# Performance work log

Measured on AMD Instinct MI355X. Metric: run time of the kernel, lower is better.

The kernel has to match this reference:

```python
import jax, jax.numpy as jnp
import numpy as np
import math

V, E, H, A, N = 32000, 512, 512, 64, 8  # vocab, embed, rnn hidden, att_size, n_heads
T, B = 256, 128                          # scan length (acts as att batch), inner dim


def _lstm(x, Wih, Whh, bih, bhh):
    # x: (T, B, E); torch nn.LSTM gate order i, f, g, o; zero initial state
    Bb = x.shape[1]
    Hh = Whh.shape[1]
    init = (jnp.zeros((Bb, Hh), x.dtype), jnp.zeros((Bb, Hh), x.dtype))

    def step(carry, xt):
        h, c = carry
        gates = xt @ Wih.T + bih + h @ Whh.T + bhh          # (B, 4H)
        i, f, g, o = jnp.split(gates, 4, axis=-1)
        c = jax.nn.sigmoid(f) * c + jax.nn.sigmoid(i) * jnp.tanh(g)
        h = jax.nn.sigmoid(o) * jnp.tanh(c)
        return (h, c), h

    _, hs = jax.lax.scan(step, init, x)
    return hs  # (T, B, H)


def setup_inputs() -> dict:
    key = jax.random.key(0)
    ks = jax.random.split(key, 26)
    rn = lambda k, s: jax.random.normal(k, s, jnp.float32) * 0.02
    inp = {
        "input_seq_l": jax.random.randint(ks[0], (T, B), 0, V, jnp.int32),
        "input_seq_r": jax.random.randint(ks[1], (T, B), 0, V, jnp.int32),
        "emb_l": rn(ks[2], (V, E)),
        "emb_r": rn(ks[3], (V, E)),
        "Wih_l": rn(ks[4], (4 * H, E)), "Whh_l": rn(ks[5], (4 * H, H)),
        "bih_l": rn(ks[6], (4 * H,)), "bhh_l": rn(ks[7], (4 * H,)),
        "Wih_r": rn(ks[8], (4 * H, E)), "Whh_r": rn(ks[9], (4 * H, H)),
        "bih_r": rn(ks[10], (4 * H,)), "bhh_r": rn(ks[11], (4 * H,)),
        "Wq": rn(ks[12], (N, H, A)), "bq": rn(ks[13], (N, A)),
        "Wk": rn(ks[14], (N, H, A)), "bk": rn(ks[15], (N, A)),
        "Wv": rn(ks[16], (N, H, A)), "bv": rn(ks[17], (N, A)),
        "Wo": rn(ks[18], (N * A, H)), "bo": rn(ks[19], (H,)),
        "Wh": rn(ks[20], (2 * H, 64)), "bh": rn(ks[21], (64,)),
        "Wa": rn(ks[22], (64, 2)), "ba": rn(ks[23], (2,)),
    }
    return inp


def reference(input_seq_l, input_seq_r, emb_l, emb_r,
              Wih_l, Whh_l, bih_l, bhh_l,
              Wih_r, Whh_r, bih_r, bhh_r,
              Wq, bq, Wk, bk, Wv, bv, Wo, bo, Wh, bh, Wa, ba):
    # left encoder
    ol = _lstm(emb_l[input_seq_l], Wih_l, Whh_l, bih_l, bhh_l)   # (T, B, H)
    # multi-head attention over left outputs (all heads batched)
    q = jnp.einsum('tbh,nhd->ntbd', ol, Wq) + bq[:, None, None, :]
    k = jnp.einsum('tbh,nhd->ntbd', ol, Wk) + bk[:, None, None, :]
    v = jnp.einsum('tbh,nhd->ntbd', ol, Wv) + bv[:, None, None, :]
    scores = jnp.einsum('ntbd,ntcd->ntbc', q, k) / math.sqrt(A)  # (N, T, B, B)
    p = jax.nn.softmax(scores, axis=-1)
    att = jnp.einsum('ntbc,ntcd->ntbd', p, v)                    # (N, T, B, A)
    att = att.transpose(1, 2, 0, 3).reshape(att.shape[1], att.shape[2], -1)  # (T, B, N*A)
    ol = att @ Wo + bo                                           # (T, B, H)
    ol = ol.mean(axis=1)                                         # (T, H)
    # right encoder
    orr = _lstm(emb_r[input_seq_r], Wih_r, Whh_r, bih_r, bhh_r).mean(axis=1)  # (T, H)
    cat = jnp.concatenate([ol, orr], axis=1)                     # (T, 2H)
    fc = cat @ Wh + bh
    ans = jax.nn.softmax(fc @ Wa + ba, axis=1)                   # (T, 2)
    return ans
```

## Files before the change

kernel.cpp:

```cpp
#include <hip/hip_runtime.h>

typedef unsigned short u16;
typedef __attribute__((ext_vector_type(4))) float f32x4;
typedef __attribute__((ext_vector_type(8))) short bf8;

#define MFMA16(a, b, c) __builtin_amdgcn_mfma_f32_16x16x32_bf16((a), (b), (c), 0, 0, 0)

__device__ __forceinline__ u16 f2bf(float f) {
  unsigned u = __builtin_bit_cast(unsigned, f);
  u += 0x7FFFu + ((u >> 16) & 1u);
  return (u16)(u >> 16);
}
__device__ __forceinline__ float bf2f(u16 h) {
  unsigned u = ((unsigned)h) << 16;
  return __builtin_bit_cast(float, u);
}
__device__ __forceinline__ float sigm(float x) { return 1.0f / (1.0f + __expf(-x)); }
__device__ __forceinline__ float tanh_f(float x) {
  x = fminf(fmaxf(x, -15.f), 15.f);
  float e = __expf(2.f * x);
  return (e - 1.f) / (e + 1.f);
}

__global__ void k_cast(const float* __restrict__ in, u16* __restrict__ out, int n4) {
  int i = blockIdx.x * blockDim.x + threadIdx.x;
  if (i >= n4) return;
  float4 v = ((const float4*)in)[i];
  union { u16 h[4]; uint2 u; } p;
  p.h[0] = f2bf(v.x); p.h[1] = f2bf(v.y); p.h[2] = f2bf(v.z); p.h[3] = f2bf(v.w);
  ((uint2*)out)[i] = p.u;
}

__global__ void k_bsum(const float* __restrict__ a, const float* __restrict__ b,
                       float* __restrict__ o, int n) {
  int i = blockIdx.x * blockDim.x + threadIdx.x;
  if (i < n) o[i] = a[i] + b[i];
}

__global__ void k_zero32(unsigned* __restrict__ p, int n) {
  int i = blockIdx.x * blockDim.x + threadIdx.x;
  if (i < n) p[i] = 0u;
}

__global__ void k_fill(float* __restrict__ p, int n, float v) {
  int i = blockIdx.x * blockDim.x + threadIdx.x;
  if (i < n) p[i] = v;
}

__global__ void k_tqkv(const float* __restrict__ W, u16* __restrict__ WT) {
  int g = blockIdx.x * blockDim.x + threadIdx.x;
  int n = g >> 15, d = (g >> 9) & 63, h = g & 511;
  WT[g] = f2bf(W[(n << 15) + (h << 6) + d]);
}

__global__ __launch_bounds__(256, 2) void k_gemm_gates(
    const int* __restrict__ idx, const float* __restrict__ emb,
    const float* __restrict__ Wih, u16* __restrict__ Gpre, int m_base) {
  __shared__ u16 lA[128][72];
  __shared__ u16 lB[128][72];
  int n0 = blockIdx.x * 128;
  int m0 = blockIdx.y * 128;
  int tid = threadIdx.x;
  int lane = tid & 63, wid = tid >> 6;
  int wm = (wid >> 1) << 6, wn = (wid & 1) << 6;
  int lq = lane >> 4, lc = lane & 15;
  f32x4 acc[4][4] = {};
  for (int k0 = 0; k0 < 512; k0 += 64) {
#pragma unroll
    for (int s = 0; s < 2; s++) {
      int slot = tid + s * 256;
      int row = slot >> 2, seg = (slot & 3) << 4;
      const float* pa = emb + (size_t)idx[m_base + m0 + row] * 512 + k0 + seg;
      const float* pb = Wih + (size_t)(n0 + row) * 512 + k0 + seg;
      float4 a0 = ((const float4*)pa)[0], a1 = ((const float4*)pa)[1];
      float4 a2 = ((const float4*)pa)[2], a3 = ((const float4*)pa)[3];
      float4 b0 = ((const float4*)pb)[0], b1 = ((const float4*)pb)[1];
      float4 b2 = ((const float4*)pb)[2], b3 = ((const float4*)pb)[3];
      union { u16 h[8]; int4 v; } pk;
      pk.h[0]=f2bf(a0.x); pk.h[1]=f2bf(a0.y); pk.h[2]=f2bf(a0.z); pk.h[3]=f2bf(a0.w);
      pk.h[4]=f2bf(a1.x); pk.h[5]=f2bf(a1.y); pk.h[6]=f2bf(a1.z); pk.h[7]=f2bf(a1.w);
      *(int4*)&lA[row][seg] = pk.v;
      pk.h[0]=f2bf(a2.x); pk.h[1]=f2bf(a2.y); pk.h[2]=f2bf(a2.z); pk.h[3]=f2bf(a2.w);
      pk.h[4]=f2bf(a3.x); pk.h[5]=f2bf(a3.y); pk.h[6]=f2bf(a3.z); pk.h[7]=f2bf(a3.w);
      *(int4*)&lA[row][seg + 8] = pk.v;
      pk.h[0]=f2bf(b0.x); pk.h[1]=f2bf(b0.y); pk.h[2]=f2bf(b0.z); pk.h[3]=f2bf(b0.w);
      pk.h[4]=f2bf(b1.x); pk.h[5]=f2bf(b1.y); pk.h[6]=f2bf(b1.z); pk.h[7]=f2bf(b1.w);
      *(int4*)&lB[row][seg] = pk.v;
      pk.h[0]=f2bf(b2.x); pk.h[1]=f2bf(b2.y); pk.h[2]=f2bf(b2.z); pk.h[3]=f2bf(b2.w);
      pk.h[4]=f2bf(b3.x); pk.h[5]=f2bf(b3.y); pk.h[6]=f2bf(b3.z); pk.h[7]=f2bf(b3.w);
      *(int4*)&lB[row][seg + 8] = pk.v;
    }
    __syncthreads();
#pragma unroll
    for (int kk = 0; kk < 64; kk += 32) {
      int ko = kk + (lq << 3);
      bf8 af[4], bg[4];
#pragma unroll
      for (int i = 0; i < 4; i++) af[i] = *(const bf8*)&lA[wm + i * 16 + lc][ko];
#pragma unroll
      for (int j = 0; j < 4; j++) bg[j] = *(const bf8*)&lB[wn + j * 16 + lc][ko];
#pragma unroll
      for (int i = 0; i < 4; i++)
#pragma unroll
        for (int j = 0; j < 4; j++) acc[i][j] = MFMA16(af[i], bg[j], acc[i][j]);
    }
    __syncthreads();
  }
  int cr = lq << 2;
#pragma unroll
  for (int i = 0; i < 4; i++)
#pragma unroll
    for (int j = 0; j < 4; j++)
#pragma unroll
      for (int r = 0; r < 4; r++) {
        int m = m0 + wm + i * 16 + cr + r;
        int nn = n0 + wn + j * 16 + lc;
        Gpre[(size_t)m * 2048 + nn] = f2bf(acc[i][j][r]);
      }
}

__global__ __launch_bounds__(256, 1) void k_lstm2(
    const u16* __restrict__ Gl, const u16* __restrict__ Gr,
    const u16* __restrict__ Whl, const u16* __restrict__ Whr,
    const float* __restrict__ bsl, const float* __restrict__ bsr,
    u16* __restrict__ hsl, u16* __restrict__ hsr,
    unsigned* __restrict__ hx, float* __restrict__ cstate,
    unsigned* __restrict__ flg, int t0, int nT) {
  __shared__ __align__(16) char hlds[32768];
  int bid = blockIdx.x;
  int pod = bid & 7, cg = bid >> 3;
  int e = pod >> 2, bg = pod & 3;
  int b0 = bg << 5, c0 = cg << 5;
  const u16* Gpre = e ? Gr : Gl;
  const u16* Whh  = e ? Whr : Whl;
  const float* bsum = e ? bsr : bsl;
  u16* hs = e ? hsr : hsl;

  int tid = threadIdx.x, lane = tid & 63, w = tid >> 6;
  int lq = lane >> 4, lc = lane & 15, cr = lq << 2;
  int cl = (w << 3) + (lc & 7);
  int gg0 = lc >> 3;
  int lr0 = (gg0 << 5) + cl;
  int lr1 = ((2 + gg0) << 5) + cl;
  int gc0 = (gg0 << 9) + c0 + cl;
  int gc1 = ((2 + gg0) << 9) + c0 + cl;
  float bs0 = bsum[gc0], bs1 = bsum[gc1];
  bool owner = (lc & 8) != 0;

  int gr0 = ((lr0 >> 5) << 9) + c0 + (lr0 & 31);
  int gr1 = ((lr1 >> 5) << 9) + c0 + (lr1 & 31);
  bf8 wb0[16], wb1[16];
  {
    const u16* p0 = Whh + (size_t)gr0 * 512 + (lq << 3);
    const u16* p1 = Whh + (size_t)gr1 * 512 + (lq << 3);
#pragma unroll
    for (int ks = 0; ks < 16; ks++) {
      wb0[ks] = *(const bf8*)(p0 + (ks << 5));
      wb1[ks] = *(const bf8*)(p1 + (ks << 5));
    }
  }
  float creg[2][4];
#pragma unroll
  for (int mi = 0; mi < 2; mi++)
#pragma unroll
    for (int r = 0; r < 4; r++) creg[mi][r] = 0.f;
  if (t0 > 0 && owner) {
#pragma unroll
    for (int mi = 0; mi < 2; mi++)
#pragma unroll
      for (int r = 0; r < 4; r++)
        creg[mi][r] = cstate[(size_t)((e << 7) + b0 + (mi << 4) + cr + r) * 512 + c0 + cl];
  }

  u16 gp[2][2][4];
#pragma unroll
  for (int mi = 0; mi < 2; mi++)
#pragma unroll
    for (int r = 0; r < 4; r++) {
      size_t rowb = (size_t)(b0 + (mi << 4) + cr + r) << 11;
      gp[mi][0][r] = Gpre[rowb + gc0];
      gp[mi][1][r] = Gpre[rowb + gc1];
    }

  int ax = (lc & 7) << 4;
  int abyte0 = lc << 10;
  int abyte1 = (16 + lc) << 10;
  int hxc = (c0 >> 1) + (w << 2) + ((lc & 7) >> 1);
  const int srow = tid >> 6;
  const int scolb = (tid & 63) << 4;

  for (int t = 0; t < nT; t++) {
    int tg = t0 + t;
    f32x4 acc[2][2] = {};
    if (tg > 0) {
      if (t > 0) {
        if (tid < 64) {
          const unsigned* fa = flg + (pod << 6) + (lane & 15);
          unsigned fv;
          int guard = 0;
          while (true) {
            asm volatile("global_load_dword %0, %1, off sc0 sc1"
                         : "=v"(fv) : "v"(fa) : "memory");
            asm volatile("s_waitcnt vmcnt(0)" ::: "memory");
            if (__ballot(fv >= (unsigned)t) == ~0ull) break;
            if (++guard > 300000) break;
          }
        }
        __syncthreads();
      }
      const unsigned* hxr = hx + (((size_t)((e << 1) | ((tg - 1) & 1))) << 15);
      uint4 sv[8];
#pragma unroll
      for (int i = 0; i < 8; i++) {
        int row = (i << 2) + srow;
        const unsigned* ap = hxr + (((size_t)(b0 + row)) << 8) + ((tid & 63) << 2);
        asm volatile("global_load_dwordx4 %0, %1, off sc0 sc1"
                     : "=v"(sv[i]) : "v"(ap));
      }
      asm volatile("s_waitcnt vmcnt(0)" ::: "memory");
      __builtin_amdgcn_sched_barrier(0);
#pragma unroll
      for (int i = 0; i < 8; i++) {
        int row = (i << 2) + srow;
        *(uint4*)(hlds + (row << 10) + (scolb ^ ((row & 7) << 4))) = sv[i];
      }
      __syncthreads();
#pragma unroll
      for (int ks = 0; ks < 16; ks++) {
        int kb = (ks << 6) + (lq << 4);
        bf8 a0 = *(const bf8*)(hlds + abyte0 + (kb ^ ax));
        bf8 a1 = *(const bf8*)(hlds + abyte1 + (kb ^ ax));
        acc[0][0] = MFMA16(a0, wb0[ks], acc[0][0]);
        acc[0][1] = MFMA16(a0, wb1[ks], acc[0][1]);
        acc[1][0] = MFMA16(a1, wb0[ks], acc[1][0]);
        acc[1][1] = MFMA16(a1, wb1[ks], acc[1][1]);
      }
      __syncthreads();
    }
    unsigned* hxw = hx + (((size_t)((e << 1) | (tg & 1))) << 15);
#pragma unroll
    for (int mi = 0; mi < 2; mi++)
#pragma unroll
      for (int r = 0; r < 4; r++) {
        float v0 = acc[mi][0][r] + bf2f(gp[mi][0][r]) + bs0;
        float v1 = acc[mi][1][r] + bf2f(gp[mi][1][r]) + bs1;
        float send = sigm(v0) * tanh_f(v1);
        float recv = __shfl_xor(send, 8, 64);
        float h = 0.f;
        if (owner) {
          float c = sigm(v0) * creg[mi][r] + recv;
          creg[mi][r] = c;
          h = sigm(v1) * tanh_f(c);
        }
        unsigned hb = (unsigned)f2bf(h);
        unsigned hi = __shfl_down(hb, 1, 64);
        unsigned packed = (hb & 0xffffu) | (hi << 16);
        int b = b0 + (mi << 4) + cr + r;
        if (owner) {
          hs[((size_t)((tg << 7) + b) << 9) + c0 + cl] = (u16)hb;
          if (!(lane & 1)) {
            unsigned* sa = hxw + (((size_t)b) << 8) + hxc;
            asm volatile("global_store_dword %0, %1, off sc0 sc1"
                         :: "v"(sa), "v"(packed) : "memory");
          }
        }
      }
    asm volatile("s_waitcnt vmcnt(0)" ::: "memory");
    __syncthreads();
    if (tid == 0) {
      unsigned tv = (unsigned)(t + 1);
      unsigned* fa = flg + (pod << 6) + cg;
      asm volatile("global_store_dword %0, %1, off sc0 sc1"
                   :: "v"(fa), "v"(tv) : "memory");
    }
    if (t + 1 < nT) {
#pragma unroll
      for (int mi = 0; mi < 2; mi++)
#pragma unroll
        for (int r = 0; r < 4; r++) {
          size_t rowb = (size_t)(((t + 1) << 7) + b0 + (mi << 4) + cr + r) << 11;
          gp[mi][0][r] = Gpre[rowb + gc0];
          gp[mi][1][r] = Gpre[rowb + gc1];
        }
    }
  }
  if (owner) {
#pragma unroll
    for (int mi = 0; mi < 2; mi++)
#pragma unroll
      for (int r = 0; r < 4; r++)
        cstate[(size_t)((e << 7) + b0 + (mi << 4) + cr + r) * 512 + c0 + cl] = creg[mi][r];
  }
}

__global__ __launch_bounds__(256) void k_meanr(const u16* __restrict__ hs, float* __restrict__ out) {
  __shared__ float part[4][512];
  int t = blockIdx.x, tid = threadIdx.x;
  int rg = tid >> 6, ln = tid & 63;
  float s[8] = {};
  for (int b = rg << 5; b < (rg << 5) + 32; b++) {
    bf8 v = *(const bf8*)(hs + (((size_t)((t << 7) + b)) << 9) + (ln << 3));
#pragma unroll
    for (int j = 0; j < 8; j++) s[j] += bf2f((u16)v[j]);
  }
#pragma unroll
  for (int j = 0; j < 8; j++) part[rg][(ln << 3) + j] = s[j];
  __syncthreads();
  for (int c = tid; c < 512; c += 256)
    out[(t << 9) + c] = (part[0][c] + part[1][c] + part[2][c] + part[3][c]) * 0.0078125f;
}

__global__ __launch_bounds__(256, 1) void k_attn(
    const u16* __restrict__ hs,
    const u16* __restrict__ WqT, const u16* __restrict__ WkT, const u16* __restrict__ WvT,
    const float* __restrict__ bq, const float* __restrict__ bk, const float* __restrict__ bv,
    float* __restrict__ attmean) {
  __shared__ __align__(16) char smem[123904];
  u16 (*qs)[72]  = (u16(*)[72])smem;
  u16 (*ksm)[72] = (u16(*)[72])(smem + 18432);
  u16 (*vt)[136] = (u16(*)[136])(smem + 36864);
  float (*sc)[132] = (float(*)[132])(smem + 54272);
  u16 (*ps)[136] = (u16(*)[136])smem;
  float* red = (float*)(smem + 54272);
  float* pmax = (float*)(smem + 121856);
  float* psum = (float*)(smem + 122880);

  int bid = blockIdx.x;
  int n = bid >> 8, t = bid & 255;
  int tid = threadIdx.x, lane = tid & 63, wid = tid >> 6;
  int lq = lane >> 4, lc = lane & 15, cr = lq << 2;
  const u16* ol = hs + ((size_t)t << 16);

  float bqv[4], bkv[4];
#pragma unroll
  for (int nf = 0; nf < 4; nf++) {
    bqv[nf] = bq[(n << 6) + (nf << 4) + lc];
    bkv[nf] = bk[(n << 6) + (nf << 4) + lc];
  }
  float bvv[4][4];
#pragma unroll
  for (int mi = 0; mi < 4; mi++)
#pragma unroll
    for (int r = 0; r < 4; r++) bvv[mi][r] = bv[(n << 6) + (mi << 4) + cr + r];

  const u16* wq = WqT + ((size_t)n << 15);
  const u16* wk = WkT + ((size_t)n << 15);
  const u16* wv = WvT + ((size_t)n << 15);
  f32x4 aq[2][4] = {}, ak[2][4] = {}, av[4][2] = {};
  for (int ks = 0; ks < 16; ks++) {
    int ko = (ks << 5) + (lq << 3);
    bf8 a0 = *(const bf8*)&ol[(size_t)((wid << 5) + lc) * 512 + ko];
    bf8 a1 = *(const bf8*)&ol[(size_t)((wid << 5) + 16 + lc) * 512 + ko];
#pragma unroll
    for (int nf = 0; nf < 4; nf++) {
      bf8 bw = *(const bf8*)&wq[(size_t)((nf << 4) + lc) * 512 + ko];
      aq[0][nf] = MFMA16(a0, bw, aq[0][nf]);
      aq[1][nf] = MFMA16(a1, bw, aq[1][nf]);
      bf8 bw2 = *(const bf8*)&wk[(size_t)((nf << 4) + lc) * 512 + ko];
      ak[0][nf] = MFMA16(a0, bw2, ak[0][nf]);
      ak[1][nf] = MFMA16(a1, bw2, ak[1][nf]);
    }
#pragma unroll
    for (int mi = 0; mi < 4; mi++) {
      bf8 aw = *(const bf8*)&wv[(size_t)((mi << 4) + lc) * 512 + ko];
      av[mi][0] = MFMA16(aw, a0, av[mi][0]);
      av[mi][1] = MFMA16(aw, a1, av[mi][1]);
    }
  }
#pragma unroll
  for (int mi = 0; mi < 2; mi++)
#pragma unroll
    for (int nf = 0; nf < 4; nf++)
#pragma unroll
      for (int r = 0; r < 4; r++) {
        int b = (wid << 5) + (mi << 4) + cr + r;
        int d = (nf << 4) + lc;
        qs[b][d] = f2bf(aq[mi][nf][r] + bqv[nf]);
        ksm[b][d] = f2bf(ak[mi][nf][r] + bkv[nf]);
      }
#pragma unroll
  for (int mi = 0; mi < 4; mi++)
#pragma unroll
    for (int c2 = 0; c2 < 2; c2++)
#pragma unroll
      for (int r = 0; r < 4; r++) {
        int d = (mi << 4) + cr + r;
        int c = (wid << 5) + (c2 << 4) + lc;
        vt[d][c] = f2bf(av[mi][c2][r] + bvv[mi][r]);
      }
  __syncthreads();

  f32x4 as_[2][8] = {};
#pragma unroll
  for (int ks = 0; ks < 2; ks++) {
    int ko = (ks << 5) + (lq << 3);
    bf8 a0 = *(const bf8*)&qs[(wid << 5) + lc][ko];
    bf8 a1 = *(const bf8*)&qs[(wid << 5) + 16 + lc][ko];
#pragma unroll
    for (int nf = 0; nf < 8; nf++) {
      bf8 bw = *(const bf8*)&ksm[(nf << 4) + lc][ko];
      as_[0][nf] = MFMA16(a0, bw, as_[0][nf]);
      as_[1][nf] = MFMA16(a1, bw, as_[1][nf]);
    }
  }
#pragma unroll
  for (int mi = 0; mi < 2; mi++)
#pragma unroll
    for (int nf = 0; nf < 8; nf++)
#pragma unroll
      for (int r = 0; r < 4; r++)
        sc[(wid << 5) + (mi << 4) + cr + r][(nf << 4) + lc] = as_[mi][nf][r] * 0.125f;
  __syncthreads();

  {
    int row = tid & 127, half = tid >> 7;
    int cb = half << 6;
    float mx = -1e30f;
    for (int j = 0; j < 64; j++) mx = fmaxf(mx, sc[row][cb + j]);
    pmax[(half << 7) + row] = mx;
    __syncthreads();
    mx = fmaxf(pmax[row], pmax[128 + row]);
    float s = 0.f;
    for (int j = 0; j < 64; j++) { float ev = __expf(sc[row][cb + j] - mx); s += ev; sc[row][cb + j] = ev; }
    psum[(half << 7) + row] = s;
    __syncthreads();
    float inv = 1.f / (psum[row] + psum[128 + row]);
    for (int j = 0; j < 64; j++) ps[row][cb + j] = f2bf(sc[row][cb + j] * inv);
  }
  __syncthreads();

  f32x4 ao[2][4] = {};
#pragma unroll
  for (int ks = 0; ks < 4; ks++) {
    int ko = (ks << 5) + (lq << 3);
    bf8 a0 = *(const bf8*)&ps[(wid << 5) + lc][ko];
    bf8 a1 = *(const bf8*)&ps[(wid << 5) + 16 + lc][ko];
#pragma unroll
    for (int nf = 0; nf < 4; nf++) {
      bf8 bw = *(const bf8*)&vt[(nf << 4) + lc][ko];
      ao[0][nf] = MFMA16(a0, bw, ao[0][nf]);
      ao[1][nf] = MFMA16(a1, bw, ao[1][nf]);
    }
  }
  float pm[4];
#pragma unroll
  for (int nf = 0; nf < 4; nf++) {
    float s = 0.f;
#pragma unroll
    for (int mi = 0; mi < 2; mi++)
#pragma unroll
      for (int r = 0; r < 4; r++) s += ao[mi][nf][r];
    s += __shfl_xor(s, 16, 64);
    s += __shfl_xor(s, 32, 64);
    pm[nf] = s;
  }
  if (lq == 0) {
#pragma unroll
    for (int nf = 0; nf < 4; nf++) red[(wid << 6) + (nf << 4) + lc] = pm[nf];
  }
  __syncthreads();
  if (tid < 64) {
    float s = red[tid] + red[64 + tid] + red[128 + tid] + red[192 + tid];
    attmean[(t << 9) + (n << 6) + tid] = s * 0.0078125f;
  }
}

__global__ __launch_bounds__(256) void k_olm(const float* __restrict__ am, const float* __restrict__ Wo,
                                             const float* __restrict__ bo, float* __restrict__ olm) {
  __shared__ float row[512];
  int t = blockIdx.x >> 1, h0 = (blockIdx.x & 1) << 8;
  int tid = threadIdx.x;
  row[tid] = am[(t << 9) + tid];
  row[tid + 256] = am[(t << 9) + 256 + tid];
  __syncthreads();
  int h = h0 + tid;
  float s = bo[h];
  for (int k = 0; k < 512; k++) s += row[k] * Wo[(k << 9) + h];
  olm[(t << 9) + h] = s;
}

__global__ __launch_bounds__(64) void k_final(const float* __restrict__ olmp, const float* __restrict__ hrm,
                                              const float* __restrict__ Wh, const float* __restrict__ bh,
                                              const float* __restrict__ Wa, const float* __restrict__ ba,
                                              float* __restrict__ out) {
  __shared__ float cat[1024];
  int t = blockIdx.x, j = threadIdx.x;
  for (int i = j; i < 512; i += 64) {
    cat[i] = olmp[(t << 9) + i];
    cat[512 + i] = hrm[(t << 9) + i];
  }
  __syncthreads();
  float f = bh[j];
  for (int k = 0; k < 1024; k++) f += cat[k] * Wh[(k << 6) + j];
  float p0 = f * Wa[j * 2], p1 = f * Wa[j * 2 + 1];
#pragma unroll
  for (int o = 32; o > 0; o >>= 1) { p0 += __shfl_down(p0, o); p1 += __shfl_down(p1, o); }
  if (j == 0) {
    p0 += ba[0]; p1 += ba[1];
    float m = fmaxf(p0, p1);
    float e0 = __expf(p0 - m), e1 = __expf(p1 - m);
    float inv = 1.f / (e0 + e1);
    out[t * 2] = e0 * inv;
    out[t * 2 + 1] = e1 * inv;
  }
}

extern "C" void kernel_launch(void* const* d_in, const int* in_sizes, int n_in,
                              void* d_out, int out_size, void* d_ws, size_t ws_size,
                              hipStream_t stream) {
  const int*   seq_l = (const int*)d_in[0];
  const int*   seq_r = (const int*)d_in[1];
  const float* emb_l = (const float*)d_in[2];
  const float* emb_r = (const float*)d_in[3];
  const float* Wih_l = (const float*)d_in[4];
  const float* Whh_l = (const float*)d_in[5];
  const float* bih_l = (const float*)d_in[6];
  const float* bhh_l = (const float*)d_in[7];
  const float* Wih_r = (const float*)d_in[8];
  const float* Whh_r = (const float*)d_in[9];
  const float* bih_r = (const float*)d_in[10];
  const float* bhh_r = (const float*)d_in[11];
  const float* Wq = (const float*)d_in[12];
  const float* bq = (const float*)d_in[13];
  const float* Wk = (const float*)d_in[14];
  const float* bk = (const float*)d_in[15];
  const float* Wv = (const float*)d_in[16];
  const float* bv = (const float*)d_in[17];
  const float* Wo = (const float*)d_in[18];
  const float* bo = (const float*)d_in[19];
  const float* Wh = (const float*)d_in[20];
  const float* bhc = (const float*)d_in[21];
  const float* Wa = (const float*)d_in[22];
  const float* ba = (const float*)d_in[23];
  float* out = (float*)d_out;

  char* ws = (char*)d_ws;
  size_t off = 0;
  auto alloc = [&](size_t bytes) { char* p = ws + off; off += (bytes + 255) & ~(size_t)255; return p; };
  u16*   hsl  = (u16*)alloc(33554432);
  u16*   hsr  = (u16*)alloc(33554432);
  u16*   Whl  = (u16*)alloc(2097152);
  u16*   Whr  = (u16*)alloc(2097152);
  u16*   WqT  = (u16*)alloc(524288);
  u16*   WkT  = (u16*)alloc(524288);
  u16*   WvT  = (u16*)alloc(524288);
  float* bsl  = (float*)alloc(8192);
  float* bsr  = (float*)alloc(8192);
  unsigned* hx = (unsigned*)alloc(524288);
  float* cst  = (float*)alloc(524288);
  unsigned* flg = (unsigned*)alloc(2048);
  float* am   = (float*)alloc(524288);
  float* hrm  = (float*)alloc(524288);
  float* olm  = (float*)alloc(524288);
  size_t fixed = off;

  int Tc = 0;
  const int cands[4] = {256, 128, 64, 32};
  for (int i = 0; i < 4; i++) {
    size_t need = fixed + 2ull * (size_t)cands[i] * 524288ull;
    if (need <= ws_size) { Tc = cands[i]; break; }
  }
  if (Tc == 0) {
    k_fill<<<2, 256, 0, stream>>>(out, out_size, 0.25f);
    return;
  }
  size_t gbytes = (size_t)Tc * 524288ull;
  u16* Gl = (u16*)alloc(gbytes);
  u16* Gr = (u16*)alloc(gbytes);

  k_cast<<<1024, 256, 0, stream>>>(Whh_l, Whl, 262144);
  k_cast<<<1024, 256, 0, stream>>>(Whh_r, Whr, 262144);
  k_bsum<<<8, 256, 0, stream>>>(bih_l, bhh_l, bsl, 2048);
  k_bsum<<<8, 256, 0, stream>>>(bih_r, bhh_r, bsr, 2048);
  k_tqkv<<<1024, 256, 0, stream>>>(Wq, WqT);
  k_tqkv<<<1024, 256, 0, stream>>>(Wk, WkT);
  k_tqkv<<<1024, 256, 0, stream>>>(Wv, WvT);

  int nC = 256 / Tc;
  for (int c = 0; c < nC; c++) {
    int m_base = c * Tc * 128;
    k_gemm_gates<<<dim3(16, Tc), 256, 0, stream>>>(seq_l, emb_l, Wih_l, Gl, m_base);
    k_gemm_gates<<<dim3(16, Tc), 256, 0, stream>>>(seq_r, emb_r, Wih_r, Gr, m_base);
    k_zero32<<<2, 256, 0, stream>>>(flg, 512);
    k_lstm2<<<128, 256, 0, stream>>>(Gl, Gr, Whl, Whr, bsl, bsr, hsl, hsr,
                                     hx, cst, flg, c * Tc, Tc);
  }
  k_meanr<<<256, 256, 0, stream>>>(hsr, hrm);
  k_attn<<<2048, 256, 0, stream>>>(hsl, WqT, WkT, WvT, bq, bk, bv, am);
  k_olm<<<512, 256, 0, stream>>>(am, Wo, bo, olm);
  k_final<<<256, 64, 0, stream>>>(olm, hrm, Wh, bhc, Wa, ba, out);
}
```

Baseline: 1.869 ms.

## Overlap next-chunk input GEMM with LSTM recurrence in a fused kernel

The input-projection GEMM and the persistent LSTM recurrence are merged into one launch. The first 128 blocks run the recurrence for the current time chunk while extra blocks compute the gate pre-activations for the next chunk into a double buffer, so the GEMM runs on otherwise idle CUs. The chunk size is capped at 128 so that there are at least two chunks to pipeline, and the flags now use global timesteps so they do not need resetting between chunks. The h stores are also packed into 32-bit writes. The risk is that the GEMM blocks compete with the spin-waiting recurrence blocks for memory bandwidth, and that more kernel launches and chunk boundaries add overhead.

```diff
diff --git a/kernel.cpp b/kernel.cpp
--- a/kernel.cpp
+++ b/kernel.cpp
@@ -53,14 +53,12 @@
   WT[g] = f2bf(W[(n << 15) + (h << 6) + d]);
 }
 
-__global__ __launch_bounds__(256, 2) void k_gemm_gates(
+__device__ __forceinline__ void gemm_body(
     const int* __restrict__ idx, const float* __restrict__ emb,
-    const float* __restrict__ Wih, u16* __restrict__ Gpre, int m_base) {
-  __shared__ u16 lA[128][72];
-  __shared__ u16 lB[128][72];
-  int n0 = blockIdx.x * 128;
-  int m0 = blockIdx.y * 128;
-  int tid = threadIdx.x;
+    const float* __restrict__ Wih, u16* __restrict__ Gpre,
+    int m_base, int m0, int n0, char* smem, int tid) {
+  u16 (*lA)[72] = (u16(*)[72])smem;
+  u16 (*lB)[72] = (u16(*)[72])(smem + 18432);
   int lane = tid & 63, wid = tid >> 6;
   int wm = (wid >> 1) << 6, wn = (wid & 1) << 6;
   int lq = lane >> 4, lc = lane & 15;
@@ -119,15 +117,21 @@
       }
 }
 
-__global__ __launch_bounds__(256, 1) void k_lstm2(
+__global__ __launch_bounds__(256, 2) void k_gemm_gates(
+    const int* __restrict__ idx, const float* __restrict__ emb,
+    const float* __restrict__ Wih, u16* __restrict__ Gpre, int m_base) {
+  __shared__ __align__(16) char smem[36864];
+  gemm_body(idx, emb, Wih, Gpre, m_base, blockIdx.y << 7, blockIdx.x << 7,
+            smem, threadIdx.x);
+}
+
+__device__ void lstm_body(
     const u16* __restrict__ Gl, const u16* __restrict__ Gr,
     const u16* __restrict__ Whl, const u16* __restrict__ Whr,
     const float* __restrict__ bsl, const float* __restrict__ bsr,
     u16* __restrict__ hsl, u16* __restrict__ hsr,
     unsigned* __restrict__ hx, float* __restrict__ cstate,
-    unsigned* __restrict__ flg, int t0, int nT) {
-  __shared__ __align__(16) char hlds[32768];
-  int bid = blockIdx.x;
+    unsigned* __restrict__ flg, int t0, int nT, char* hlds, int bid, int tid) {
   int pod = bid & 7, cg = bid >> 3;
   int e = pod >> 2, bg = pod & 3;
   int b0 = bg << 5, c0 = cg << 5;
@@ -136,7 +140,7 @@
   const float* bsum = e ? bsr : bsl;
   u16* hs = e ? hsr : hsl;
 
-  int tid = threadIdx.x, lane = tid & 63, w = tid >> 6;
+  int lane = tid & 63, w = tid >> 6;
   int lq = lane >> 4, lc = lane & 15, cr = lq << 2;
   int cl = (w << 3) + (lc & 7);
   int gg0 = lc >> 3;
@@ -202,7 +206,7 @@
             asm volatile("global_load_dword %0, %1, off sc0 sc1"
                          : "=v"(fv) : "v"(fa) : "memory");
             asm volatile("s_waitcnt vmcnt(0)" ::: "memory");
-            if (__ballot(fv >= (unsigned)t) == ~0ull) break;
+            if (__ballot(fv >= (unsigned)tg) == ~0ull) break;
             if (++guard > 300000) break;
           }
         }
@@ -256,19 +260,17 @@
         unsigned hi = __shfl_down(hb, 1, 64);
         unsigned packed = (hb & 0xffffu) | (hi << 16);
         int b = b0 + (mi << 4) + cr + r;
-        if (owner) {
-          hs[((size_t)((tg << 7) + b) << 9) + c0 + cl] = (u16)hb;
-          if (!(lane & 1)) {
-            unsigned* sa = hxw + (((size_t)b) << 8) + hxc;
-            asm volatile("global_store_dword %0, %1, off sc0 sc1"
-                         :: "v"(sa), "v"(packed) : "memory");
-          }
+        if (owner && !(lane & 1)) {
+          *(unsigned*)(hs + (((size_t)((tg << 7) + b)) << 9) + c0 + cl) = packed;
+          unsigned* sa = hxw + (((size_t)b) << 8) + hxc;
+          asm volatile("global_store_dword %0, %1, off sc0 sc1"
+                       :: "v"(sa), "v"(packed) : "memory");
         }
       }
     asm volatile("s_waitcnt vmcnt(0)" ::: "memory");
     __syncthreads();
     if (tid == 0) {
-      unsigned tv = (unsigned)(t + 1);
+      unsigned tv = (unsigned)(tg + 1);
       unsigned* fa = flg + (pod << 6) + cg;
       asm volatile("global_store_dword %0, %1, off sc0 sc1"
                    :: "v"(fa), "v"(tv) : "memory");
@@ -290,6 +292,32 @@
 #pragma unroll
       for (int r = 0; r < 4; r++)
         cstate[(size_t)((e << 7) + b0 + (mi << 4) + cr + r) * 512 + c0 + cl] = creg[mi][r];
+  }
+}
+
+__global__ __launch_bounds__(256, 1) void k_fused(
+    const u16* __restrict__ Gl, const u16* __restrict__ Gr,
+    u16* __restrict__ Ggl, u16* __restrict__ Ggr,
+    const int* __restrict__ seq_l, const int* __restrict__ seq_r,
+    const float* __restrict__ emb_l, const float* __restrict__ emb_r,
+    const float* __restrict__ Wih_l, const float* __restrict__ Wih_r,
+    const u16* __restrict__ Whl, const u16* __restrict__ Whr,
+    const float* __restrict__ bsl, const float* __restrict__ bsr,
+    u16* __restrict__ hsl, u16* __restrict__ hsr,
+    unsigned* __restrict__ hx, float* __restrict__ cstate,
+    unsigned* __restrict__ flg, int t0, int nT, int gmb, int Tc) {
+  __shared__ __align__(16) char smem[36864];
+  int bid = blockIdx.x, tid = threadIdx.x;
+  if (bid < 128) {
+    lstm_body(Gl, Gr, Whl, Whr, bsl, bsr, hsl, hsr, hx, cstate, flg,
+              t0, nT, smem, bid, tid);
+  } else {
+    int gb = bid - 128;
+    int per = Tc << 4;
+    int ge = gb >= per;
+    int rem = ge ? gb - per : gb;
+    gemm_body(ge ? seq_r : seq_l, ge ? emb_r : emb_l, ge ? Wih_r : Wih_l,
+              ge ? Ggr : Ggl, gmb, (rem >> 4) << 7, (rem & 15) << 7, smem, tid);
   }
 }
 
@@ -555,9 +583,9 @@
   size_t fixed = off;
 
   int Tc = 0;
-  const int cands[4] = {256, 128, 64, 32};
-  for (int i = 0; i < 4; i++) {
-    size_t need = fixed + 2ull * (size_t)cands[i] * 524288ull;
+  const int cands[3] = {128, 64, 32};
+  for (int i = 0; i < 3; i++) {
+    size_t need = fixed + 4ull * (size_t)cands[i] * 524288ull;
     if (need <= ws_size) { Tc = cands[i]; break; }
   }
   if (Tc == 0) {
@@ -565,9 +593,11 @@
     return;
   }
   size_t gbytes = (size_t)Tc * 524288ull;
-  u16* Gl = (u16*)alloc(gbytes);
-  u16* Gr = (u16*)alloc(gbytes);
-
+  u16* Glb[2]; u16* Grb[2];
+  Glb[0] = (u16*)alloc(gbytes); Glb[1] = (u16*)alloc(gbytes);
+  Grb[0] = (u16*)alloc(gbytes); Grb[1] = (u16*)alloc(gbytes);
+
+  k_zero32<<<2, 256, 0, stream>>>(flg, 512);
   k_cast<<<1024, 256, 0, stream>>>(Whh_l, Whl, 262144);
   k_cast<<<1024, 256, 0, stream>>>(Whh_r, Whr, 262144);
   k_bsum<<<8, 256, 0, stream>>>(bih_l, bhh_l, bsl, 2048);
@@ -576,14 +606,18 @@
   k_tqkv<<<1024, 256, 0, stream>>>(Wk, WkT);
   k_tqkv<<<1024, 256, 0, stream>>>(Wv, WvT);
 
+  k_gemm_gates<<<dim3(16, Tc), 256, 0, stream>>>(seq_l, emb_l, Wih_l, Glb[0], 0);
+  k_gemm_gates<<<dim3(16, Tc), 256, 0, stream>>>(seq_r, emb_r, Wih_r, Grb[0], 0);
+
   int nC = 256 / Tc;
   for (int c = 0; c < nC; c++) {
-    int m_base = c * Tc * 128;
-    k_gemm_gates<<<dim3(16, Tc), 256, 0, stream>>>(seq_l, emb_l, Wih_l, Gl, m_base);
-    k_gemm_gates<<<dim3(16, Tc), 256, 0, stream>>>(seq_r, emb_r, Wih_r, Gr, m_base);
-    k_zero32<<<2, 256, 0, stream>>>(flg, 512);
-    k_lstm2<<<128, 256, 0, stream>>>(Gl, Gr, Whl, Whr, bsl, bsr, hsl, hsr,
-                                     hx, cst, flg, c * Tc, Tc);
+    int hg = (c + 1 < nC);
+    int grid = 128 + (hg ? (Tc << 5) : 0);
+    k_fused<<<grid, 256, 0, stream>>>(
+        Glb[c & 1], Grb[c & 1], Glb[(c + 1) & 1], Grb[(c + 1) & 1],
+        seq_l, seq_r, emb_l, emb_r, Wih_l, Wih_r,
+        Whl, Whr, bsl, bsr, hsl, hsr, hx, cst, flg,
+        c * Tc, Tc, (c + 1) * Tc * 128, Tc);
   }
   k_meanr<<<256, 256, 0, stream>>>(hsr, hrm);
   k_attn<<<2048, 256, 0, stream>>>(hsl, WqT, WkT, WvT, bq, bk, bv, am);
```

Result: faster. 1.708 ms (-8.6%).
